# Kernel optimization log

Hardware: AMD Instinct MI355X
Metric: run time of the kernel (lower is better)

The kernel has to match this reference:

```python
import jax, jax.numpy as jnp
import numpy as np

DROPOUT_RATE = 0.5
CONF_THRESH = 0.85
IGNORE_VALUE = 2
EPS = 1e-07


def setup_inputs() -> dict:
    key = jax.random.key(0)
    k1, k2 = jax.random.split(key)
    B, H, W = 16, 1024, 1024
    pred = jax.random.uniform(k1, (B, H, W), dtype=jnp.float32)
    mask = jax.random.randint(k2, (B, H, W), 0, 3, dtype=jnp.int32)
    return {"pred": pred, "mask": mask}


def _training_need_score(pred, gt, confidence):
    # Higher = needs more training: CW=4, UW=3, UC=2, CC=1 (+/- confidence bonus)
    is_correct = (pred > 0.5) == (gt == 1.0)
    is_conf = confidence > CONF_THRESH
    score = jnp.where(is_conf & is_correct, 1.0,
            jnp.where(~is_conf & is_correct, 2.0,
            jnp.where(~is_conf & ~is_correct, 3.0, 4.0))).astype(pred.dtype)
    bonus = (confidence - 0.5) * 0.5
    return jnp.where(is_correct, score - bonus, score + bonus)


def _dynamic_masks(pred, mask):
    # Vectorized equivalent of the per-batch nonzero/argsort/scatter loop:
    # rank annotated pixels per batch by descending need-score; top n_train -> train.
    B, H, W = mask.shape
    annotated = (mask != IGNORE_VALUE).reshape(B, H * W)
    gt = mask.astype(pred.dtype)
    confidence = jnp.maximum(pred, 1.0 - pred)
    scores = _training_need_score(pred, gt, confidence).reshape(B, H * W)
    neg_inf = jnp.asarray(-jnp.inf, scores.dtype)
    masked_scores = jnp.where(annotated, scores, neg_inf)
    order = jnp.argsort(-masked_scores, axis=1)          # descending score order
    rank = jnp.argsort(order, axis=1)                    # rank of each pixel in that order
    n_points = annotated.sum(axis=1)
    n_train = (n_points.astype(jnp.float32) * (1.0 - DROPOUT_RATE)).astype(jnp.int32)
    train = annotated & (rank < n_train[:, None])
    holdout = annotated & ~train
    return train.reshape(B, H, W), holdout.reshape(B, H, W)


def reference(pred, mask):
    if pred.ndim == 4 and pred.shape[1] == 1:
        pred = pred[:, 0]
    train_mask, holdout_mask = _dynamic_masks(pred, mask)
    gt = mask.astype(pred.dtype)
    p = jnp.clip(pred, EPS, 1.0 - EPS)
    bce = -(gt * jnp.log(p) + (1.0 - gt) * jnp.log(1.0 - p))
    tm = train_mask.astype(pred.dtype)
    loss = (bce * tm).sum() / (tm.sum() + EPS)
    return loss, train_mask, holdout_mask
```

## Files before the change

kernel.cpp:

```cpp
#include <hip/hip_runtime.h>
#include <stdint.h>

#define NBATCH 16
#define HW_ (1 << 20)
#define TPB 256

#define NBPB_H 32
#define TPB_H 1024
#define EPB_H (HW_ / NBPB_H)
#define ITER_H (EPB_H / (TPB_H * 4))

#define NBINS 8192
#define FBASE 0x3F400

#define TPB_RF 1024

#define NBPB_F 256
#define FCHUNK (HW_ / NBPB_F)

#define CAND_CAP 32768
#define LCAP 512
#define TIE_CAP 4096
#define CNT_STRIDE 64

typedef float f4v __attribute__((ext_vector_type(4)));

struct BParams {
    unsigned int k;
    unsigned int bin1f;
    unsigned int r;
    unsigned int mode;
};

__device__ __forceinline__ unsigned int score_bits(float p, int m) {
    bool correct = (p > 0.5f) == (m == 1);
    float conf = fmaxf(p, 1.0f - p);
    float base = correct ? ((conf > 0.85f) ? 1.0f : 2.0f)
                         : ((conf > 0.85f) ? 4.0f : 3.0f);
    float bonus = (conf - 0.5f) * 0.5f;
    float s = correct ? (base - bonus) : (base + bonus);
    return __float_as_uint(s);
}

__device__ __forceinline__ float agent_load_f32(const float* p) {
    return __hip_atomic_load(p, __ATOMIC_RELAXED, __HIP_MEMORY_SCOPE_AGENT);
}

__global__ void k_hist1(const float4* __restrict__ pred4, const int4* __restrict__ mask4,
                        unsigned int* __restrict__ hist_part16) {
    __shared__ unsigned int lh[NBINS];
    int b = blockIdx.x / NBPB_H;
    int blk = blockIdx.x % NBPB_H;
    int t = threadIdx.x;
    for (int i = t; i < NBINS; i += TPB_H) lh[i] = 0;
    __syncthreads();
    size_t gb = (size_t)b * (HW_ / 4) + (size_t)blk * (EPB_H / 4);
    float4 p = pred4[gb + t];
    int4 m = mask4[gb + t];
#pragma unroll
    for (int j = 0; j < ITER_H; j++) {
        float4 pc = p;
        int4 mc = m;
        if (j + 1 < ITER_H) {
            p = pred4[gb + (size_t)(j + 1) * TPB_H + t];
            m = mask4[gb + (size_t)(j + 1) * TPB_H + t];
        }
        float pa[4] = {pc.x, pc.y, pc.z, pc.w};
        int ma[4] = {mc.x, mc.y, mc.z, mc.w};
#pragma unroll
        for (int l = 0; l < 4; l++) {
            if (ma[l] != 2) {
                unsigned int sb = score_bits(pa[l], ma[l]);
                int fb = (int)(sb >> 12) - FBASE;
                fb = min(max(fb, 0), NBINS - 1);
                atomicAdd(&lh[fb], 1u);
            }
        }
    }
    __syncthreads();
    unsigned int* hp = hist_part16 + (size_t)(b * NBPB_H + blk) * (NBINS / 2);
    for (int w = t; w < NBINS / 2; w += TPB_H)
        hp[w] = (lh[2 * w] & 0xFFFFu) | (lh[2 * w + 1] << 16);
}

__global__ void k_redfind(const unsigned int* __restrict__ hist_part16,
                          BParams* __restrict__ prm) {
    int b = blockIdx.x;
    int t = threadIdx.x;
    __shared__ unsigned int cs_[TPB_RF + 1];
    unsigned int c[8];
#pragma unroll
    for (int j = 0; j < 8; j++) c[j] = 0;
#pragma unroll
    for (int p = 0; p < NBPB_H; p++) {
        const uint4* hp = (const uint4*)(hist_part16 + (size_t)(b * NBPB_H + p) * (NBINS / 2));
        uint4 w = hp[t];
        c[0] += w.x & 0xFFFFu; c[1] += w.x >> 16;
        c[2] += w.y & 0xFFFFu; c[3] += w.y >> 16;
        c[4] += w.z & 0xFFFFu; c[5] += w.z >> 16;
        c[6] += w.w & 0xFFFFu; c[7] += w.w >> 16;
    }
    unsigned int s = 0;
#pragma unroll
    for (int j = 0; j < 8; j++) s += c[j];
    cs_[t] = s;
    if (t == 0) cs_[TPB_RF] = 0;
    __syncthreads();
    for (int off = 1; off < TPB_RF; off <<= 1) {
        unsigned int a = (t + off < TPB_RF) ? cs_[t + off] : 0u;
        __syncthreads();
        cs_[t] += a;
        __syncthreads();
    }
    unsigned int n = cs_[0];
    unsigned int k = (unsigned int)(int)((float)n * 0.5f);
    if (k == 0) {
        if (t == 0) {
            BParams P;
            P.k = 0; P.bin1f = 0xFFFFFFFFu; P.r = 0; P.mode = 0;
            prm[b] = P;
        }
        return;
    }
    if (cs_[t] >= k && cs_[t + 1] < k) {
        unsigned int cum = cs_[t + 1];
#pragma unroll
        for (int j = 7; j >= 0; j--) {
            unsigned int hb = c[j];
            if (cum + hb >= k) {
                BParams P;
                P.k = k;
                P.bin1f = (unsigned int)(FBASE + t * 8 + j);
                P.r = k - cum;
                P.mode = 1;
                prm[b] = P;
                break;
            }
            cum += hb;
        }
    }
}

__global__ void k_main(const float4* __restrict__ pred4, const int4* __restrict__ mask4,
                       const BParams* __restrict__ prm, float* __restrict__ out,
                       float* __restrict__ partials, unsigned int* __restrict__ cand_cnt,
                       unsigned int* __restrict__ cand_idx, unsigned int* __restrict__ cand_sb,
                       float* __restrict__ cand_bce) {
    int b = blockIdx.x / NBPB_F;
    int blk = blockIdx.x % NBPB_F;
    BParams P = prm[b];
    unsigned int target = P.bin1f;
    __shared__ unsigned int lcode[FCHUNK / 4];
    __shared__ float red[TPB];
    __shared__ unsigned int l_idx[LCAP];
    __shared__ unsigned int l_sb[LCAP];
    __shared__ float l_bce[LCAP];
    __shared__ unsigned int lcnt;
    __shared__ unsigned int gbase;
    if (threadIdx.x == 0) lcnt = 0;
    __syncthreads();
    float acc = 0.0f;
    int ibase = blk * FCHUNK;
    size_t base4 = (size_t)b * (HW_ / 4) + (size_t)(ibase / 4);
    float* trout = out + 1;
    float* hoout = out + 1 + (size_t)NBATCH * HW_;
    size_t Gbase = (size_t)b * HW_ + (size_t)ibase;
    int lane = threadIdx.x & 63;
    float4 p = pred4[base4 + threadIdx.x];
    int4 m = mask4[base4 + threadIdx.x];
#pragma unroll
    for (int j = 0; j < FCHUNK / (TPB * 4); j++) {
        int v = j * TPB + threadIdx.x;
        float4 pc = p;
        int4 mc = m;
        if (j + 1 < FCHUNK / (TPB * 4)) {
            p = pred4[base4 + (size_t)(j + 1) * TPB + threadIdx.x];
            m = mask4[base4 + (size_t)(j + 1) * TPB + threadIdx.x];
        }
        float pa[4] = {pc.x, pc.y, pc.z, pc.w};
        int ma[4] = {mc.x, mc.y, mc.z, mc.w};
        unsigned int cw = 0;
#pragma unroll
        for (int l = 0; l < 4; l++) {
            bool ann = (ma[l] != 2);
            unsigned int sb = score_bits(pa[l], ma[l]);
            unsigned int fine = sb >> 12;
            bool tr = ann && (fine > target);
            bool amb = ann && (fine == target);
            unsigned int code = (tr ? 1u : 0u) | ((ann && !tr) ? 2u : 0u);
            cw |= code << (8 * l);
            float bce = 0.0f;
            if (tr || amb) {
                float pc2 = fminf(fmaxf(pa[l], 1e-7f), 1.0f - 1e-7f);
                bce = (ma[l] == 1) ? -__logf(pc2) : -__logf(1.0f - pc2);
            }
            if (tr) acc += bce;
            if (amb) {
                unsigned int p0 = atomicAdd(&lcnt, 1u);
                if (p0 < LCAP) {
                    l_idx[p0] = (unsigned int)(ibase + v * 4 + l);
                    l_sb[p0] = sb;
                    l_bce[p0] = bce;
                } else {
                    unsigned int gp = atomicAdd(&cand_cnt[b * CNT_STRIDE], 1u);
                    if (gp < CAND_CAP) {
                        size_t o = (size_t)b * CAND_CAP + gp;
                        cand_idx[o] = (unsigned int)(ibase + v * 4 + l);
                        cand_sb[o] = sb;
                        cand_bce[o] = bce;
                    }
                }
            }
        }
        lcode[v] = cw;
        unsigned int nw = (unsigned int)__shfl_down((int)cw, 1);
        if (lane != 63) {
            unsigned int c0 = cw >> 24;
            unsigned int c1 = nw & 0xFFu;
            unsigned int c2 = (nw >> 8) & 0xFFu;
            unsigned int c3 = (nw >> 16) & 0xFFu;
            int e = 3 + 4 * v;
            f4v tv = { (float)(c0 & 1u), (float)(c1 & 1u), (float)(c2 & 1u), (float)(c3 & 1u) };
            f4v hv = { (float)((c0 >> 1) & 1u), (float)((c1 >> 1) & 1u),
                       (float)((c2 >> 1) & 1u), (float)((c3 >> 1) & 1u) };
            *(f4v*)(trout + Gbase + e) = tv;
            *(f4v*)(hoout + Gbase + e) = hv;
        }
    }
    __syncthreads();
    unsigned int n = min(lcnt, (unsigned int)LCAP);
    if (threadIdx.x == 0 && n > 0)
        gbase = atomicAdd(&cand_cnt[b * CNT_STRIDE], n);
    __syncthreads();
    for (unsigned int i = threadIdx.x; i < n; i += TPB) {
        unsigned int pos = gbase + i;
        if (pos < CAND_CAP) {
            size_t o = (size_t)b * CAND_CAP + pos;
            cand_idx[o] = l_idx[i];
            cand_sb[o] = l_sb[i];
            cand_bce[o] = l_bce[i];
        }
    }
    if (threadIdx.x < 16) {
        int j = threadIdx.x >> 2, w = threadIdx.x & 3;
        int v = j * TPB + w * 64 + 63;
        if (v < FCHUNK / 4 - 1) {
            unsigned int w0 = lcode[v];
            unsigned int w1 = lcode[v + 1];
            unsigned int c0 = w0 >> 24;
            unsigned int c1 = w1 & 0xFFu;
            unsigned int c2 = (w1 >> 8) & 0xFFu;
            unsigned int c3 = (w1 >> 16) & 0xFFu;
            int e = 3 + 4 * v;
            f4v tv = { (float)(c0 & 1u), (float)(c1 & 1u), (float)(c2 & 1u), (float)(c3 & 1u) };
            f4v hv = { (float)((c0 >> 1) & 1u), (float)((c1 >> 1) & 1u),
                       (float)((c2 >> 1) & 1u), (float)((c3 >> 1) & 1u) };
            *(f4v*)(trout + Gbase + e) = tv;
            *(f4v*)(hoout + Gbase + e) = hv;
        }
    }
    if (threadIdx.x >= 16 && threadIdx.x < 19) {
        int i = threadIdx.x - 16;
        unsigned int c = (lcode[0] >> (8 * i)) & 0xFFu;
        trout[Gbase + i] = (float)(c & 1u);
        hoout[Gbase + i] = (float)((c >> 1) & 1u);
    }
    if (threadIdx.x == 19) {
        unsigned int c = (lcode[FCHUNK / 4 - 1] >> 24) & 0xFFu;
        trout[Gbase + FCHUNK - 1] = (float)(c & 1u);
        hoout[Gbase + FCHUNK - 1] = (float)((c >> 1) & 1u);
    }
    red[threadIdx.x] = acc;
    __syncthreads();
    for (int off = TPB / 2; off > 0; off >>= 1) {
        if (threadIdx.x < off) red[threadIdx.x] += red[threadIdx.x + off];
        __syncthreads();
    }
    if (threadIdx.x == 0) partials[blockIdx.x] = red[0];
}

__global__ void k_fixup(const unsigned int* __restrict__ cand_cnt,
                        const unsigned int* __restrict__ cand_idx,
                        const unsigned int* __restrict__ cand_sb,
                        const float* __restrict__ cand_bce,
                        const BParams* __restrict__ prm, float* __restrict__ out,
                        float* __restrict__ tie_partials,
                        const float* __restrict__ partials,
                        unsigned int* __restrict__ done_f) {
    int b = blockIdx.x;
    int t = threadIdx.x;
    __shared__ unsigned int h[4096];
    __shared__ unsigned int cs_[257];
    __shared__ unsigned int tie_idx[TIE_CAP];
    __shared__ unsigned int misc[8];
    __shared__ float red[TPB];
    __shared__ double redd[TPB];
    __shared__ unsigned int lastf;
    BParams P = prm[b];
    float tieval = 0.0f;
    if (P.mode != 0) {
        unsigned int C = cand_cnt[b * CNT_STRIDE];
        if (C > CAND_CAP) C = CAND_CAP;
        const unsigned int* ci = cand_idx + (size_t)b * CAND_CAP;
        const unsigned int* cs = cand_sb + (size_t)b * CAND_CAP;
        const float* cb = cand_bce + (size_t)b * CAND_CAP;
        for (int i = t; i < 4096; i += TPB) h[i] = 0;
        if (t < 8) misc[t] = (t == 4) ? 0xFFFFFFFFu : 0u;
        __syncthreads();
        for (unsigned int i = t; i < C; i += TPB)
            atomicAdd(&h[cs[i] & 0xFFFu], 1u);
        __syncthreads();
        {
            unsigned int gs = 0;
#pragma unroll
            for (int j = 0; j < 16; j++) gs += h[t * 16 + j];
            cs_[t] = gs;
            if (t == 0) cs_[256] = 0;
        }
        __syncthreads();
        for (int off = 1; off < 256; off <<= 1) {
            unsigned int a = (t + off < 256) ? cs_[t + off] : 0u;
            __syncthreads();
            cs_[t] += a;
            __syncthreads();
        }
        if (cs_[t] >= P.r && cs_[t + 1] < P.r) {
            unsigned int cum = cs_[t + 1];
            for (int j = 15; j >= 0; j--) {
                unsigned int hb = h[t * 16 + j];
                if (cum + hb >= P.r) {
                    unsigned int T = P.r - cum;
                    misc[0] = (unsigned int)(t * 16 + j);
                    misc[1] = T;
                    misc[2] = (T == hb) ? 1u : 0u;
                    break;
                }
                cum += hb;
            }
        }
        __syncthreads();
        unsigned int vstar = misc[0], T = misc[1];
        bool allTies = (misc[2] != 0);
        unsigned int idxcut;
        if (allTies) {
            idxcut = 0xFFFFFFFFu;
        } else {
            for (unsigned int i = t; i < C; i += TPB) {
                if ((cs[i] & 0xFFFu) == vstar) {
                    unsigned int p = atomicAdd(&misc[3], 1u);
                    if (p < TIE_CAP) tie_idx[p] = ci[i];
                }
            }
            __syncthreads();
            unsigned int E2 = misc[3];
            if (E2 > TIE_CAP) E2 = TIE_CAP;
            for (unsigned int i = t; i < E2; i += TPB) {
                unsigned int vi = tie_idx[i];
                unsigned int cnt = 0;
                for (unsigned int j = 0; j < E2; j++) cnt += (tie_idx[j] < vi) ? 1u : 0u;
                if (cnt == T - 1) misc[4] = vi;
            }
            __syncthreads();
            idxcut = misc[4];
        }
        float acc = 0.0f;
        float* trout = out + 1;
        float* hoout = out + 1 + (size_t)NBATCH * HW_;
        size_t base = (size_t)b * HW_;
        for (unsigned int i = t; i < C; i += TPB) {
            unsigned int low = cs[i] & 0xFFFu;
            bool tr = (low > vstar) || (low == vstar && ci[i] <= idxcut);
            if (tr) {
                trout[base + ci[i]] = 1.0f;
                hoout[base + ci[i]] = 0.0f;
                acc += cb[i];
            }
        }
        red[t] = acc;
        __syncthreads();
        for (int off = TPB / 2; off > 0; off >>= 1) {
            if (t < off) red[t] += red[t + off];
            __syncthreads();
        }
        if (t == 0) tieval = red[0];
    }
    if (t == 0)
        __hip_atomic_store(&tie_partials[b], tieval, __ATOMIC_RELAXED, __HIP_MEMORY_SCOPE_AGENT);
    __threadfence();
    __syncthreads();
    if (t == 0) lastf = (atomicAdd(done_f, 1u) == (unsigned int)(NBATCH - 1)) ? 1u : 0u;
    __syncthreads();
    if (!lastf) return;
    __threadfence();
    double s = 0.0;
    for (int i = t; i < NBATCH * NBPB_F; i += TPB) s += (double)partials[i];
    if (t < NBATCH) s += (double)agent_load_f32(&tie_partials[t]);
    redd[t] = s;
    __syncthreads();
    for (int off = TPB / 2; off > 0; off >>= 1) {
        if (t < off) redd[t] += redd[t + off];
        __syncthreads();
    }
    if (t == 0) {
        unsigned long long den = 0;
        for (int b2 = 0; b2 < NBATCH; b2++) den += prm[b2].k;
        float denf = (float)den + 1e-7f;
        out[0] = (float)redd[0] / denf;
    }
}

extern "C" void kernel_launch(void* const* d_in, const int* in_sizes, int n_in,
                              void* d_out, int out_size, void* d_ws, size_t ws_size,
                              hipStream_t stream) {
    const float4* pred4 = (const float4*)d_in[0];
    const int4* mask4 = (const int4*)d_in[1];
    float* out = (float*)d_out;

    unsigned int* cand_cnt = (unsigned int*)d_ws;
    unsigned int* done_f = cand_cnt + NBATCH * CNT_STRIDE;
    BParams* prm = (BParams*)(done_f + 32);
    float* partials = (float*)(prm + NBATCH);
    float* tie_partials = partials + NBATCH * NBPB_F;
    unsigned int* cand_idx = (unsigned int*)(tie_partials + NBATCH);
    unsigned int* cand_sb = cand_idx + NBATCH * CAND_CAP;
    float* cand_bce = (float*)(cand_sb + NBATCH * CAND_CAP);
    unsigned int* hist_part16 = (unsigned int*)(cand_bce + NBATCH * CAND_CAP);

    size_t zero_bytes = (size_t)(NBATCH * CNT_STRIDE + 32) * 4;
    hipMemsetAsync(d_ws, 0, zero_bytes, stream);

    k_hist1<<<dim3(NBATCH * NBPB_H), dim3(TPB_H), 0, stream>>>(pred4, mask4, hist_part16);
    k_redfind<<<dim3(NBATCH), dim3(TPB_RF), 0, stream>>>(hist_part16, prm);
    k_main<<<dim3(NBATCH * NBPB_F), dim3(TPB), 0, stream>>>(pred4, mask4, prm, out, partials,
                                                            cand_cnt, cand_idx, cand_sb, cand_bce);
    k_fixup<<<dim3(NBATCH), dim3(TPB), 0, stream>>>(cand_cnt, cand_idx, cand_sb, cand_bce,
                                                    prm, out, tie_partials, partials, done_f);
}
```

Measured before the change: 295.4 us.

## Fuse four kernel launches into one cooperative persistent kernel with grid syncs

Merges the histogram, threshold-finding, main masking, and tie fixup kernels into one cooperative kernel of 512 blocks with 512 threads, separated by grid.sync barriers. The histogram reduction is parallelized across slices, and the memset is replaced by in-kernel zeroing. This aims to remove launch gaps and the memset. It reduces the main-pass grid from 4096 blocks to 512 and adds several grid-wide barriers, which can hurt latency hiding.

```diff
diff --git a/kernel.cpp b/kernel.cpp
--- a/kernel.cpp
+++ b/kernel.cpp
@@ -1,27 +1,28 @@
 #include <hip/hip_runtime.h>
+#include <hip/hip_cooperative_groups.h>
 #include <stdint.h>
+
+namespace cg = cooperative_groups;
 
 #define NBATCH 16
 #define HW_ (1 << 20)
-#define TPB 256
-
-#define NBPB_H 32
-#define TPB_H 1024
-#define EPB_H (HW_ / NBPB_H)
-#define ITER_H (EPB_H / (TPB_H * 4))
+#define NB 512
+#define TPBC 512
+#define NBPB 32
+#define EPB (HW_ / NBPB)
+#define ITER_P (EPB / (TPBC * 4))
 
 #define NBINS 8192
 #define FBASE 0x3F400
-
-#define TPB_RF 1024
-
-#define NBPB_F 256
-#define FCHUNK (HW_ / NBPB_F)
+#define NSLICE 32
+#define SLICE_BINS 256
 
 #define CAND_CAP 32768
 #define LCAP 512
 #define TIE_CAP 4096
 #define CNT_STRIDE 64
+
+#define BUF_W 10242
 
 typedef float f4v __attribute__((ext_vector_type(4)));
 
@@ -42,209 +43,212 @@
     return __float_as_uint(s);
 }
 
-__device__ __forceinline__ float agent_load_f32(const float* p) {
-    return __hip_atomic_load(p, __ATOMIC_RELAXED, __HIP_MEMORY_SCOPE_AGENT);
-}
-
-__global__ void k_hist1(const float4* __restrict__ pred4, const int4* __restrict__ mask4,
-                        unsigned int* __restrict__ hist_part16) {
-    __shared__ unsigned int lh[NBINS];
-    int b = blockIdx.x / NBPB_H;
-    int blk = blockIdx.x % NBPB_H;
-    int t = threadIdx.x;
-    for (int i = t; i < NBINS; i += TPB_H) lh[i] = 0;
+__global__ __launch_bounds__(TPBC, 4) void k_all(
+    const float4* __restrict__ pred4, const int4* __restrict__ mask4,
+    float* __restrict__ out,
+    unsigned int* __restrict__ cand_cnt, BParams* __restrict__ prm,
+    float* __restrict__ partials, float* __restrict__ tie_partials,
+    unsigned int* __restrict__ cand_idx, unsigned int* __restrict__ cand_sb,
+    float* __restrict__ cand_bce, unsigned int* __restrict__ hist1,
+    unsigned int* __restrict__ stot, unsigned int* __restrict__ hist_part16)
+{
+    cg::grid_group grid = cg::this_grid();
+    __shared__ __align__(16) unsigned int buf[BUF_W];
+    const int blk = blockIdx.x;
+    const int t = threadIdx.x;
+    const int b = blk / NBPB;
+    const int sb = blk % NBPB;
+    const int lane = t & 63;
+
+    for (int i = t; i < NBINS; i += TPBC) buf[i] = 0;
+    if (blk == 0)
+        for (int i = t; i < NBATCH * CNT_STRIDE; i += TPBC) cand_cnt[i] = 0;
     __syncthreads();
-    size_t gb = (size_t)b * (HW_ / 4) + (size_t)blk * (EPB_H / 4);
-    float4 p = pred4[gb + t];
-    int4 m = mask4[gb + t];
+    {
+        size_t gb = (size_t)b * (HW_ / 4) + (size_t)sb * (EPB / 4);
+        float4 p = pred4[gb + t];
+        int4 m = mask4[gb + t];
+        for (int j = 0; j < ITER_P; j++) {
+            float4 pc = p; int4 mc = m;
+            if (j + 1 < ITER_P) {
+                p = pred4[gb + (size_t)(j + 1) * TPBC + t];
+                m = mask4[gb + (size_t)(j + 1) * TPBC + t];
+            }
+            float pa[4] = {pc.x, pc.y, pc.z, pc.w};
+            int   ma[4] = {mc.x, mc.y, mc.z, mc.w};
 #pragma unroll
-    for (int j = 0; j < ITER_H; j++) {
-        float4 pc = p;
-        int4 mc = m;
-        if (j + 1 < ITER_H) {
-            p = pred4[gb + (size_t)(j + 1) * TPB_H + t];
-            m = mask4[gb + (size_t)(j + 1) * TPB_H + t];
-        }
-        float pa[4] = {pc.x, pc.y, pc.z, pc.w};
-        int ma[4] = {mc.x, mc.y, mc.z, mc.w};
-#pragma unroll
-        for (int l = 0; l < 4; l++) {
-            if (ma[l] != 2) {
-                unsigned int sb = score_bits(pa[l], ma[l]);
-                int fb = (int)(sb >> 12) - FBASE;
-                fb = min(max(fb, 0), NBINS - 1);
-                atomicAdd(&lh[fb], 1u);
+            for (int l = 0; l < 4; l++) {
+                if (ma[l] != 2) {
+                    unsigned int sbit = score_bits(pa[l], ma[l]);
+                    int fb = (int)(sbit >> 12) - FBASE;
+                    fb = min(max(fb, 0), NBINS - 1);
+                    atomicAdd(&buf[fb], 1u);
+                }
             }
         }
     }
     __syncthreads();
-    unsigned int* hp = hist_part16 + (size_t)(b * NBPB_H + blk) * (NBINS / 2);
-    for (int w = t; w < NBINS / 2; w += TPB_H)
-        hp[w] = (lh[2 * w] & 0xFFFFu) | (lh[2 * w + 1] << 16);
-}
-
-__global__ void k_redfind(const unsigned int* __restrict__ hist_part16,
-                          BParams* __restrict__ prm) {
-    int b = blockIdx.x;
-    int t = threadIdx.x;
-    __shared__ unsigned int cs_[TPB_RF + 1];
-    unsigned int c[8];
-#pragma unroll
-    for (int j = 0; j < 8; j++) c[j] = 0;
-#pragma unroll
-    for (int p = 0; p < NBPB_H; p++) {
-        const uint4* hp = (const uint4*)(hist_part16 + (size_t)(b * NBPB_H + p) * (NBINS / 2));
-        uint4 w = hp[t];
-        c[0] += w.x & 0xFFFFu; c[1] += w.x >> 16;
-        c[2] += w.y & 0xFFFFu; c[3] += w.y >> 16;
-        c[4] += w.z & 0xFFFFu; c[5] += w.z >> 16;
-        c[6] += w.w & 0xFFFFu; c[7] += w.w >> 16;
-    }
-    unsigned int s = 0;
-#pragma unroll
-    for (int j = 0; j < 8; j++) s += c[j];
-    cs_[t] = s;
-    if (t == 0) cs_[TPB_RF] = 0;
+    {
+        unsigned int* hp = hist_part16 + (size_t)blk * (NBINS / 2);
+        for (int w = t; w < NBINS / 2; w += TPBC)
+            hp[w] = (buf[2 * w] & 0xFFFFu) | (buf[2 * w + 1] << 16);
+    }
+    grid.sync();
+
+    if (t < 128) {
+        unsigned int s0 = 0, s1 = 0;
+        for (int p = 0; p < NBPB; p++) {
+            unsigned int w = hist_part16[(size_t)(b * NBPB + p) * (NBINS / 2) + sb * 128 + t];
+            s0 += w & 0xFFFFu; s1 += w >> 16;
+        }
+        hist1[(size_t)b * NBINS + sb * SLICE_BINS + 2 * t] = s0;
+        hist1[(size_t)b * NBINS + sb * SLICE_BINS + 2 * t + 1] = s1;
+        buf[t] = s0 + s1;
+    }
     __syncthreads();
-    for (int off = 1; off < TPB_RF; off <<= 1) {
-        unsigned int a = (t + off < TPB_RF) ? cs_[t + off] : 0u;
-        __syncthreads();
-        cs_[t] += a;
-        __syncthreads();
-    }
-    unsigned int n = cs_[0];
-    unsigned int k = (unsigned int)(int)((float)n * 0.5f);
-    if (k == 0) {
+    for (int off = 64; off > 0; off >>= 1) {
+        if (t < off) buf[t] += buf[t + off];
+        __syncthreads();
+    }
+    if (t == 0) stot[b * NBPB + sb] = buf[0];
+    grid.sync();
+
+    if (sb == 0) {
+        if (t < NSLICE) buf[256 + t] = stot[b * NBPB + t];
+        __syncthreads();
         if (t == 0) {
-            BParams P;
-            P.k = 0; P.bin1f = 0xFFFFFFFFu; P.r = 0; P.mode = 0;
-            prm[b] = P;
-        }
-        return;
-    }
-    if (cs_[t] >= k && cs_[t + 1] < k) {
-        unsigned int cum = cs_[t + 1];
-#pragma unroll
-        for (int j = 7; j >= 0; j--) {
-            unsigned int hb = c[j];
-            if (cum + hb >= k) {
-                BParams P;
-                P.k = k;
-                P.bin1f = (unsigned int)(FBASE + t * 8 + j);
-                P.r = k - cum;
+            unsigned int run = 0;
+            for (int i = NSLICE - 1; i >= 0; i--) { run += buf[256 + i]; buf[288 + i] = run; }
+            buf[320] = run;
+        }
+        __syncthreads();
+        unsigned int n = buf[320];
+        unsigned int k = (unsigned int)(int)((float)n * 0.5f);
+        if (k == 0) {
+            if (t == 0) { BParams P; P.k = 0; P.bin1f = 0xFFFFFFFFu; P.r = 0; P.mode = 0; prm[b] = P; }
+        } else {
+            if (t == 0) {
+                int ss = 0;
+                for (int i = NSLICE - 1; i >= 0; i--) {
+                    unsigned int sufi = buf[288 + i];
+                    unsigned int sufn = (i == NSLICE - 1) ? 0u : buf[288 + i + 1];
+                    if (sufi >= k && sufn < k) { ss = i; break; }
+                }
+                buf[321] = (unsigned int)ss;
+                buf[322] = k - ((ss == NSLICE - 1) ? 0u : buf[288 + ss + 1]);
+            }
+            __syncthreads();
+            unsigned int ss = buf[321], rs = buf[322];
+            if (t < SLICE_BINS) buf[512 + t] = hist1[(size_t)b * NBINS + ss * SLICE_BINS + t];
+            if (t == 0) buf[512 + SLICE_BINS] = 0;
+            __syncthreads();
+            for (int off = 1; off < SLICE_BINS; off <<= 1) {
+                unsigned int a = (t < SLICE_BINS && t + off < SLICE_BINS) ? buf[512 + t + off] : 0u;
+                __syncthreads();
+                if (t < SLICE_BINS) buf[512 + t] += a;
+                __syncthreads();
+            }
+            if (t < SLICE_BINS && buf[512 + t] >= rs && buf[512 + t + 1] < rs) {
+                BParams P; P.k = k;
+                P.bin1f = (unsigned int)(FBASE + ss * SLICE_BINS + t);
+                P.r = rs - buf[512 + t + 1];
                 P.mode = 1;
                 prm[b] = P;
-                break;
-            }
-            cum += hb;
-        }
-    }
-}
-
-__global__ void k_main(const float4* __restrict__ pred4, const int4* __restrict__ mask4,
-                       const BParams* __restrict__ prm, float* __restrict__ out,
-                       float* __restrict__ partials, unsigned int* __restrict__ cand_cnt,
-                       unsigned int* __restrict__ cand_idx, unsigned int* __restrict__ cand_sb,
-                       float* __restrict__ cand_bce) {
-    int b = blockIdx.x / NBPB_F;
-    int blk = blockIdx.x % NBPB_F;
-    BParams P = prm[b];
-    unsigned int target = P.bin1f;
-    __shared__ unsigned int lcode[FCHUNK / 4];
-    __shared__ float red[TPB];
-    __shared__ unsigned int l_idx[LCAP];
-    __shared__ unsigned int l_sb[LCAP];
-    __shared__ float l_bce[LCAP];
-    __shared__ unsigned int lcnt;
-    __shared__ unsigned int gbase;
-    if (threadIdx.x == 0) lcnt = 0;
-    __syncthreads();
-    float acc = 0.0f;
-    int ibase = blk * FCHUNK;
-    size_t base4 = (size_t)b * (HW_ / 4) + (size_t)(ibase / 4);
-    float* trout = out + 1;
-    float* hoout = out + 1 + (size_t)NBATCH * HW_;
-    size_t Gbase = (size_t)b * HW_ + (size_t)ibase;
-    int lane = threadIdx.x & 63;
-    float4 p = pred4[base4 + threadIdx.x];
-    int4 m = mask4[base4 + threadIdx.x];
+            }
+        }
+    }
+    grid.sync();
+
+    {
+        unsigned int* lcode = buf;
+        unsigned int* l_idx = buf + 8192;
+        unsigned int* l_sbv = buf + 8704;
+        float*        l_bce = (float*)(buf + 9216);
+        float*        redf  = (float*)(buf + 9728);
+        BParams P = prm[b];
+        unsigned int target = P.bin1f;
+        if (t == 0) buf[10240] = 0;
+        __syncthreads();
+        float acc = 0.0f;
+        int ibase = sb * EPB;
+        size_t base4 = (size_t)b * (HW_ / 4) + (size_t)(ibase / 4);
+        float* trout = out + 1;
+        float* hoout = out + 1 + (size_t)NBATCH * HW_;
+        size_t Gbase = (size_t)b * HW_ + (size_t)ibase;
+        float4 p = pred4[base4 + t];
+        int4 m = mask4[base4 + t];
+        for (int j = 0; j < ITER_P; j++) {
+            int v = j * TPBC + t;
+            float4 pc = p; int4 mc = m;
+            if (j + 1 < ITER_P) {
+                p = pred4[base4 + (size_t)(j + 1) * TPBC + t];
+                m = mask4[base4 + (size_t)(j + 1) * TPBC + t];
+            }
+            float pa[4] = {pc.x, pc.y, pc.z, pc.w};
+            int   ma[4] = {mc.x, mc.y, mc.z, mc.w};
+            unsigned int cw = 0;
 #pragma unroll
-    for (int j = 0; j < FCHUNK / (TPB * 4); j++) {
-        int v = j * TPB + threadIdx.x;
-        float4 pc = p;
-        int4 mc = m;
-        if (j + 1 < FCHUNK / (TPB * 4)) {
-            p = pred4[base4 + (size_t)(j + 1) * TPB + threadIdx.x];
-            m = mask4[base4 + (size_t)(j + 1) * TPB + threadIdx.x];
-        }
-        float pa[4] = {pc.x, pc.y, pc.z, pc.w};
-        int ma[4] = {mc.x, mc.y, mc.z, mc.w};
-        unsigned int cw = 0;
-#pragma unroll
-        for (int l = 0; l < 4; l++) {
-            bool ann = (ma[l] != 2);
-            unsigned int sb = score_bits(pa[l], ma[l]);
-            unsigned int fine = sb >> 12;
-            bool tr = ann && (fine > target);
-            bool amb = ann && (fine == target);
-            unsigned int code = (tr ? 1u : 0u) | ((ann && !tr) ? 2u : 0u);
-            cw |= code << (8 * l);
-            float bce = 0.0f;
-            if (tr || amb) {
-                float pc2 = fminf(fmaxf(pa[l], 1e-7f), 1.0f - 1e-7f);
-                bce = (ma[l] == 1) ? -__logf(pc2) : -__logf(1.0f - pc2);
-            }
-            if (tr) acc += bce;
-            if (amb) {
-                unsigned int p0 = atomicAdd(&lcnt, 1u);
-                if (p0 < LCAP) {
-                    l_idx[p0] = (unsigned int)(ibase + v * 4 + l);
-                    l_sb[p0] = sb;
-                    l_bce[p0] = bce;
-                } else {
-                    unsigned int gp = atomicAdd(&cand_cnt[b * CNT_STRIDE], 1u);
-                    if (gp < CAND_CAP) {
-                        size_t o = (size_t)b * CAND_CAP + gp;
-                        cand_idx[o] = (unsigned int)(ibase + v * 4 + l);
-                        cand_sb[o] = sb;
-                        cand_bce[o] = bce;
+            for (int l = 0; l < 4; l++) {
+                bool ann = (ma[l] != 2);
+                unsigned int sbit = score_bits(pa[l], ma[l]);
+                unsigned int fine = sbit >> 12;
+                bool tr = ann && (fine > target);
+                bool amb = ann && (fine == target);
+                unsigned int code = (tr ? 1u : 0u) | ((ann && !tr) ? 2u : 0u);
+                cw |= code << (8 * l);
+                float bce = 0.0f;
+                if (tr || amb) {
+                    float pc2 = fminf(fmaxf(pa[l], 1e-7f), 1.0f - 1e-7f);
+                    bce = (ma[l] == 1) ? -__logf(pc2) : -__logf(1.0f - pc2);
+                }
+                if (tr) acc += bce;
+                if (amb) {
+                    unsigned int p0 = atomicAdd(&buf[10240], 1u);
+                    if (p0 < LCAP) {
+                        l_idx[p0] = (unsigned int)(ibase + v * 4 + l);
+                        l_sbv[p0] = sbit;
+                        l_bce[p0] = bce;
+                    } else {
+                        unsigned int gp = atomicAdd(&cand_cnt[b * CNT_STRIDE], 1u);
+                        if (gp < CAND_CAP) {
+                            size_t o = (size_t)b * CAND_CAP + gp;
+                            cand_idx[o] = (unsigned int)(ibase + v * 4 + l);
+                            cand_sb[o] = sbit;
+                            cand_bce[o] = bce;
+                        }
                     }
                 }
             }
-        }
-        lcode[v] = cw;
-        unsigned int nw = (unsigned int)__shfl_down((int)cw, 1);
-        if (lane != 63) {
-            unsigned int c0 = cw >> 24;
-            unsigned int c1 = nw & 0xFFu;
-            unsigned int c2 = (nw >> 8) & 0xFFu;
-            unsigned int c3 = (nw >> 16) & 0xFFu;
-            int e = 3 + 4 * v;
-            f4v tv = { (float)(c0 & 1u), (float)(c1 & 1u), (float)(c2 & 1u), (float)(c3 & 1u) };
-            f4v hv = { (float)((c0 >> 1) & 1u), (float)((c1 >> 1) & 1u),
-                       (float)((c2 >> 1) & 1u), (float)((c3 >> 1) & 1u) };
-            *(f4v*)(trout + Gbase + e) = tv;
-            *(f4v*)(hoout + Gbase + e) = hv;
-        }
-    }
-    __syncthreads();
-    unsigned int n = min(lcnt, (unsigned int)LCAP);
-    if (threadIdx.x == 0 && n > 0)
-        gbase = atomicAdd(&cand_cnt[b * CNT_STRIDE], n);
-    __syncthreads();
-    for (unsigned int i = threadIdx.x; i < n; i += TPB) {
-        unsigned int pos = gbase + i;
-        if (pos < CAND_CAP) {
-            size_t o = (size_t)b * CAND_CAP + pos;
-            cand_idx[o] = l_idx[i];
-            cand_sb[o] = l_sb[i];
-            cand_bce[o] = l_bce[i];
-        }
-    }
-    if (threadIdx.x < 16) {
-        int j = threadIdx.x >> 2, w = threadIdx.x & 3;
-        int v = j * TPB + w * 64 + 63;
-        if (v < FCHUNK / 4 - 1) {
+            lcode[v] = cw;
+            unsigned int nw = (unsigned int)__shfl_down((int)cw, 1);
+            if (lane != 63) {
+                unsigned int c0 = cw >> 24;
+                unsigned int c1 = nw & 0xFFu;
+                unsigned int c2 = (nw >> 8) & 0xFFu;
+                unsigned int c3 = (nw >> 16) & 0xFFu;
+                int e = 3 + 4 * v;
+                f4v tv = { (float)(c0 & 1u), (float)(c1 & 1u), (float)(c2 & 1u), (float)(c3 & 1u) };
+                f4v hv = { (float)((c0 >> 1) & 1u), (float)((c1 >> 1) & 1u),
+                           (float)((c2 >> 1) & 1u), (float)((c3 >> 1) & 1u) };
+                *(f4v*)(trout + Gbase + e) = tv;
+                *(f4v*)(hoout + Gbase + e) = hv;
+            }
+        }
+        __syncthreads();
+        unsigned int ncand = min(buf[10240], (unsigned int)LCAP);
+        if (t == 0 && ncand > 0) buf[10241] = atomicAdd(&cand_cnt[b * CNT_STRIDE], ncand);
+        __syncthreads();
+        for (unsigned int i = t; i < ncand; i += TPBC) {
+            unsigned int pos = buf[10241] + i;
+            if (pos < CAND_CAP) {
+                size_t o = (size_t)b * CAND_CAP + pos;
+                cand_idx[o] = l_idx[i];
+                cand_sb[o] = l_sbv[i];
+                cand_bce[o] = l_bce[i];
+            }
+        }
+        if (t < 127) {
+            int v = t * 64 + 63;
             unsigned int w0 = lcode[v];
             unsigned int w1 = lcode[v + 1];
             unsigned int c0 = w0 >> 24;
@@ -258,154 +262,140 @@
             *(f4v*)(trout + Gbase + e) = tv;
             *(f4v*)(hoout + Gbase + e) = hv;
         }
-    }
-    if (threadIdx.x >= 16 && threadIdx.x < 19) {
-        int i = threadIdx.x - 16;
-        unsigned int c = (lcode[0] >> (8 * i)) & 0xFFu;
-        trout[Gbase + i] = (float)(c & 1u);
-        hoout[Gbase + i] = (float)((c >> 1) & 1u);
-    }
-    if (threadIdx.x == 19) {
-        unsigned int c = (lcode[FCHUNK / 4 - 1] >> 24) & 0xFFu;
-        trout[Gbase + FCHUNK - 1] = (float)(c & 1u);
-        hoout[Gbase + FCHUNK - 1] = (float)((c >> 1) & 1u);
-    }
-    red[threadIdx.x] = acc;
-    __syncthreads();
-    for (int off = TPB / 2; off > 0; off >>= 1) {
-        if (threadIdx.x < off) red[threadIdx.x] += red[threadIdx.x + off];
-        __syncthreads();
-    }
-    if (threadIdx.x == 0) partials[blockIdx.x] = red[0];
-}
-
-__global__ void k_fixup(const unsigned int* __restrict__ cand_cnt,
-                        const unsigned int* __restrict__ cand_idx,
-                        const unsigned int* __restrict__ cand_sb,
-                        const float* __restrict__ cand_bce,
-                        const BParams* __restrict__ prm, float* __restrict__ out,
-                        float* __restrict__ tie_partials,
-                        const float* __restrict__ partials,
-                        unsigned int* __restrict__ done_f) {
-    int b = blockIdx.x;
-    int t = threadIdx.x;
-    __shared__ unsigned int h[4096];
-    __shared__ unsigned int cs_[257];
-    __shared__ unsigned int tie_idx[TIE_CAP];
-    __shared__ unsigned int misc[8];
-    __shared__ float red[TPB];
-    __shared__ double redd[TPB];
-    __shared__ unsigned int lastf;
-    BParams P = prm[b];
-    float tieval = 0.0f;
-    if (P.mode != 0) {
-        unsigned int C = cand_cnt[b * CNT_STRIDE];
-        if (C > CAND_CAP) C = CAND_CAP;
-        const unsigned int* ci = cand_idx + (size_t)b * CAND_CAP;
-        const unsigned int* cs = cand_sb + (size_t)b * CAND_CAP;
-        const float* cb = cand_bce + (size_t)b * CAND_CAP;
-        for (int i = t; i < 4096; i += TPB) h[i] = 0;
-        if (t < 8) misc[t] = (t == 4) ? 0xFFFFFFFFu : 0u;
-        __syncthreads();
-        for (unsigned int i = t; i < C; i += TPB)
-            atomicAdd(&h[cs[i] & 0xFFFu], 1u);
-        __syncthreads();
-        {
-            unsigned int gs = 0;
+        if (t >= 128 && t < 131) {
+            int i = t - 128;
+            unsigned int c = (lcode[0] >> (8 * i)) & 0xFFu;
+            trout[Gbase + i] = (float)(c & 1u);
+            hoout[Gbase + i] = (float)((c >> 1) & 1u);
+        }
+        if (t == 131) {
+            unsigned int c = (lcode[EPB / 4 - 1] >> 24) & 0xFFu;
+            trout[Gbase + EPB - 1] = (float)(c & 1u);
+            hoout[Gbase + EPB - 1] = (float)((c >> 1) & 1u);
+        }
+        redf[t] = acc;
+        __syncthreads();
+        for (int off = TPBC / 2; off > 0; off >>= 1) {
+            if (t < off) redf[t] += redf[t + off];
+            __syncthreads();
+        }
+        if (t == 0) partials[blk] = redf[0];
+    }
+    grid.sync();
+
+    if (sb == 0) {
+        unsigned int* h    = buf;
+        unsigned int* csx  = buf + 4096;
+        unsigned int* tie  = buf + 4609;
+        unsigned int* misc = buf + 8705;
+        float* redf = (float*)(buf + 8713);
+        BParams P = prm[b];
+        if (P.mode == 0) {
+            if (t == 0) tie_partials[b] = 0.0f;
+        } else {
+            unsigned int C = cand_cnt[b * CNT_STRIDE];
+            if (C > CAND_CAP) C = CAND_CAP;
+            const unsigned int* ci = cand_idx + (size_t)b * CAND_CAP;
+            const unsigned int* cs = cand_sb + (size_t)b * CAND_CAP;
+            const float* cb = cand_bce + (size_t)b * CAND_CAP;
+            for (int i = t; i < 4096; i += TPBC) h[i] = 0;
+            if (t < 8) misc[t] = (t == 4) ? 0xFFFFFFFFu : 0u;
+            __syncthreads();
+            for (unsigned int i = t; i < C; i += TPBC)
+                atomicAdd(&h[cs[i] & 0xFFFu], 1u);
+            __syncthreads();
+            {
+                unsigned int gs = 0;
 #pragma unroll
-            for (int j = 0; j < 16; j++) gs += h[t * 16 + j];
-            cs_[t] = gs;
-            if (t == 0) cs_[256] = 0;
-        }
-        __syncthreads();
-        for (int off = 1; off < 256; off <<= 1) {
-            unsigned int a = (t + off < 256) ? cs_[t + off] : 0u;
-            __syncthreads();
-            cs_[t] += a;
-            __syncthreads();
-        }
-        if (cs_[t] >= P.r && cs_[t + 1] < P.r) {
-            unsigned int cum = cs_[t + 1];
-            for (int j = 15; j >= 0; j--) {
-                unsigned int hb = h[t * 16 + j];
-                if (cum + hb >= P.r) {
-                    unsigned int T = P.r - cum;
-                    misc[0] = (unsigned int)(t * 16 + j);
-                    misc[1] = T;
-                    misc[2] = (T == hb) ? 1u : 0u;
-                    break;
-                }
-                cum += hb;
-            }
-        }
-        __syncthreads();
-        unsigned int vstar = misc[0], T = misc[1];
-        bool allTies = (misc[2] != 0);
-        unsigned int idxcut;
-        if (allTies) {
-            idxcut = 0xFFFFFFFFu;
-        } else {
-            for (unsigned int i = t; i < C; i += TPB) {
-                if ((cs[i] & 0xFFFu) == vstar) {
-                    unsigned int p = atomicAdd(&misc[3], 1u);
-                    if (p < TIE_CAP) tie_idx[p] = ci[i];
-                }
-            }
-            __syncthreads();
-            unsigned int E2 = misc[3];
-            if (E2 > TIE_CAP) E2 = TIE_CAP;
-            for (unsigned int i = t; i < E2; i += TPB) {
-                unsigned int vi = tie_idx[i];
-                unsigned int cnt = 0;
-                for (unsigned int j = 0; j < E2; j++) cnt += (tie_idx[j] < vi) ? 1u : 0u;
-                if (cnt == T - 1) misc[4] = vi;
-            }
-            __syncthreads();
-            idxcut = misc[4];
-        }
-        float acc = 0.0f;
-        float* trout = out + 1;
-        float* hoout = out + 1 + (size_t)NBATCH * HW_;
-        size_t base = (size_t)b * HW_;
-        for (unsigned int i = t; i < C; i += TPB) {
-            unsigned int low = cs[i] & 0xFFFu;
-            bool tr = (low > vstar) || (low == vstar && ci[i] <= idxcut);
-            if (tr) {
-                trout[base + ci[i]] = 1.0f;
-                hoout[base + ci[i]] = 0.0f;
-                acc += cb[i];
-            }
-        }
-        red[t] = acc;
-        __syncthreads();
-        for (int off = TPB / 2; off > 0; off >>= 1) {
-            if (t < off) red[t] += red[t + off];
-            __syncthreads();
-        }
-        if (t == 0) tieval = red[0];
-    }
-    if (t == 0)
-        __hip_atomic_store(&tie_partials[b], tieval, __ATOMIC_RELAXED, __HIP_MEMORY_SCOPE_AGENT);
-    __threadfence();
-    __syncthreads();
-    if (t == 0) lastf = (atomicAdd(done_f, 1u) == (unsigned int)(NBATCH - 1)) ? 1u : 0u;
-    __syncthreads();
-    if (!lastf) return;
-    __threadfence();
-    double s = 0.0;
-    for (int i = t; i < NBATCH * NBPB_F; i += TPB) s += (double)partials[i];
-    if (t < NBATCH) s += (double)agent_load_f32(&tie_partials[t]);
-    redd[t] = s;
-    __syncthreads();
-    for (int off = TPB / 2; off > 0; off >>= 1) {
-        if (t < off) redd[t] += redd[t + off];
-        __syncthreads();
-    }
-    if (t == 0) {
-        unsigned long long den = 0;
-        for (int b2 = 0; b2 < NBATCH; b2++) den += prm[b2].k;
-        float denf = (float)den + 1e-7f;
-        out[0] = (float)redd[0] / denf;
+                for (int j = 0; j < 8; j++) gs += h[t * 8 + j];
+                csx[t] = gs;
+                if (t == 0) csx[TPBC] = 0;
+            }
+            __syncthreads();
+            for (int off = 1; off < TPBC; off <<= 1) {
+                unsigned int a = (t + off < TPBC) ? csx[t + off] : 0u;
+                __syncthreads();
+                csx[t] += a;
+                __syncthreads();
+            }
+            if (csx[t] >= P.r && csx[t + 1] < P.r) {
+                unsigned int cum = csx[t + 1];
+                for (int j = 7; j >= 0; j--) {
+                    unsigned int hb = h[t * 8 + j];
+                    if (cum + hb >= P.r) {
+                        unsigned int T = P.r - cum;
+                        misc[0] = (unsigned int)(t * 8 + j);
+                        misc[1] = T;
+                        misc[2] = (T == hb) ? 1u : 0u;
+                        break;
+                    }
+                    cum += hb;
+                }
+            }
+            __syncthreads();
+            unsigned int vstar = misc[0], T = misc[1];
+            bool allTies = (misc[2] != 0);
+            unsigned int idxcut;
+            if (allTies) {
+                idxcut = 0xFFFFFFFFu;
+            } else {
+                for (unsigned int i = t; i < C; i += TPBC) {
+                    if ((cs[i] & 0xFFFu) == vstar) {
+                        unsigned int p0 = atomicAdd(&misc[3], 1u);
+                        if (p0 < TIE_CAP) tie[p0] = ci[i];
+                    }
+                }
+                __syncthreads();
+                unsigned int E2 = misc[3];
+                if (E2 > TIE_CAP) E2 = TIE_CAP;
+                for (unsigned int i = t; i < E2; i += TPBC) {
+                    unsigned int vi = tie[i];
+                    unsigned int cnt = 0;
+                    for (unsigned int j2 = 0; j2 < E2; j2++) cnt += (tie[j2] < vi) ? 1u : 0u;
+                    if (cnt == T - 1) misc[4] = vi;
+                }
+                __syncthreads();
+                idxcut = misc[4];
+            }
+            float accd = 0.0f;
+            float* trout = out + 1;
+            float* hoout = out + 1 + (size_t)NBATCH * HW_;
+            size_t baseo = (size_t)b * HW_;
+            for (unsigned int i = t; i < C; i += TPBC) {
+                unsigned int low = cs[i] & 0xFFFu;
+                bool tr = (low > vstar) || (low == vstar && ci[i] <= idxcut);
+                if (tr) {
+                    trout[baseo + ci[i]] = 1.0f;
+                    hoout[baseo + ci[i]] = 0.0f;
+                    accd += cb[i];
+                }
+            }
+            redf[t] = accd;
+            __syncthreads();
+            for (int off = TPBC / 2; off > 0; off >>= 1) {
+                if (t < off) redf[t] += redf[t + off];
+                __syncthreads();
+            }
+            if (t == 0) tie_partials[b] = redf[0];
+        }
+    }
+    grid.sync();
+
+    if (blk == 0) {
+        double* redd = (double*)buf;
+        double s = (double)partials[t];
+        if (t < NBATCH) s += (double)tie_partials[t];
+        redd[t] = s;
+        __syncthreads();
+        for (int off = TPBC / 2; off > 0; off >>= 1) {
+            if (t < off) redd[t] += redd[t + off];
+            __syncthreads();
+        }
+        if (t == 0) {
+            unsigned long long den = 0;
+            for (int b2 = 0; b2 < NBATCH; b2++) den += prm[b2].k;
+            out[0] = (float)redd[0] / ((float)den + 1e-7f);
+        }
     }
 }
 
@@ -417,22 +407,19 @@
     float* out = (float*)d_out;
 
     unsigned int* cand_cnt = (unsigned int*)d_ws;
-    unsigned int* done_f = cand_cnt + NBATCH * CNT_STRIDE;
-    BParams* prm = (BParams*)(done_f + 32);
+    BParams* prm = (BParams*)(cand_cnt + NBATCH * CNT_STRIDE);
     float* partials = (float*)(prm + NBATCH);
-    float* tie_partials = partials + NBATCH * NBPB_F;
-    unsigned int* cand_idx = (unsigned int*)(tie_partials + NBATCH);
+    float* tie_partials = partials + NB;
+    unsigned int* stot = (unsigned int*)(tie_partials + NBATCH);
+    unsigned int* cand_idx = stot + NB;
     unsigned int* cand_sb = cand_idx + NBATCH * CAND_CAP;
     float* cand_bce = (float*)(cand_sb + NBATCH * CAND_CAP);
-    unsigned int* hist_part16 = (unsigned int*)(cand_bce + NBATCH * CAND_CAP);
-
-    size_t zero_bytes = (size_t)(NBATCH * CNT_STRIDE + 32) * 4;
-    hipMemsetAsync(d_ws, 0, zero_bytes, stream);
-
-    k_hist1<<<dim3(NBATCH * NBPB_H), dim3(TPB_H), 0, stream>>>(pred4, mask4, hist_part16);
-    k_redfind<<<dim3(NBATCH), dim3(TPB_RF), 0, stream>>>(hist_part16, prm);
-    k_main<<<dim3(NBATCH * NBPB_F), dim3(TPB), 0, stream>>>(pred4, mask4, prm, out, partials,
-                                                            cand_cnt, cand_idx, cand_sb, cand_bce);
-    k_fixup<<<dim3(NBATCH), dim3(TPB), 0, stream>>>(cand_cnt, cand_idx, cand_sb, cand_bce,
-                                                    prm, out, tie_partials, partials, done_f);
+    unsigned int* hist1 = (unsigned int*)(cand_bce + NBATCH * CAND_CAP);
+    unsigned int* hist_part16 = hist1 + NBATCH * NBINS;
+
+    void* args[] = { (void*)&pred4, (void*)&mask4, (void*)&out, (void*)&cand_cnt,
+                     (void*)&prm, (void*)&partials, (void*)&tie_partials,
+                     (void*)&cand_idx, (void*)&cand_sb, (void*)&cand_bce,
+                     (void*)&hist1, (void*)&stot, (void*)&hist_part16 };
+    hipLaunchCooperativeKernel((const void*)k_all, dim3(NB), dim3(TPBC), args, 0, stream);
 }
```

New measurement: 564.8 us. 1.91x slower.

## Split histogram reduce/find into parallel kernels and retune histogram blocks

Applied to the files above, without the earlier changes.

Doubles the number of histogram blocks per batch and halves their size, with a launch bound and a two-deep load prefetch. The former single-block-per-batch reduce-and-scan kernel becomes a sliced reduction kernel with 64 blocks plus a smaller 256-thread find kernel that scans the reduced histogram. The aim is to spread the partial-histogram reduction over more CUs and raise occupancy in the histogram pass. The cost is an extra kernel launch, twice as many partial histograms to write and read, and a serial 32-bin scan in the find step.

```diff
diff --git a/kernel.cpp b/kernel.cpp
--- a/kernel.cpp
+++ b/kernel.cpp
@@ -5,15 +5,16 @@
 #define HW_ (1 << 20)
 #define TPB 256
 
-#define NBPB_H 32
-#define TPB_H 1024
+#define NBPB_H 64
+#define TPB_H 512
 #define EPB_H (HW_ / NBPB_H)
 #define ITER_H (EPB_H / (TPB_H * 4))
 
 #define NBINS 8192
 #define FBASE 0x3F400
 
-#define TPB_RF 1024
+#define NSLICE 4
+#define SLICE_W (NBINS / 2 / NSLICE)
 
 #define NBPB_F 256
 #define FCHUNK (HW_ / NBPB_F)
@@ -46,8 +47,9 @@
     return __hip_atomic_load(p, __ATOMIC_RELAXED, __HIP_MEMORY_SCOPE_AGENT);
 }
 
-__global__ void k_hist1(const float4* __restrict__ pred4, const int4* __restrict__ mask4,
-                        unsigned int* __restrict__ hist_part16) {
+__global__ __launch_bounds__(TPB_H, 8) void k_hist1(
+        const float4* __restrict__ pred4, const int4* __restrict__ mask4,
+        unsigned int* __restrict__ hist_part16) {
     __shared__ unsigned int lh[NBINS];
     int b = blockIdx.x / NBPB_H;
     int blk = blockIdx.x % NBPB_H;
@@ -55,16 +57,7 @@
     for (int i = t; i < NBINS; i += TPB_H) lh[i] = 0;
     __syncthreads();
     size_t gb = (size_t)b * (HW_ / 4) + (size_t)blk * (EPB_H / 4);
-    float4 p = pred4[gb + t];
-    int4 m = mask4[gb + t];
-#pragma unroll
-    for (int j = 0; j < ITER_H; j++) {
-        float4 pc = p;
-        int4 mc = m;
-        if (j + 1 < ITER_H) {
-            p = pred4[gb + (size_t)(j + 1) * TPB_H + t];
-            m = mask4[gb + (size_t)(j + 1) * TPB_H + t];
-        }
+    auto process = [&](float4 pc, int4 mc) {
         float pa[4] = {pc.x, pc.y, pc.z, pc.w};
         int ma[4] = {mc.x, mc.y, mc.z, mc.w};
 #pragma unroll
@@ -76,6 +69,25 @@
                 atomicAdd(&lh[fb], 1u);
             }
         }
+    };
+    float4 p0 = pred4[gb + t];
+    int4 m0 = mask4[gb + t];
+    float4 p1 = pred4[gb + TPB_H + t];
+    int4 m1 = mask4[gb + TPB_H + t];
+#pragma unroll
+    for (int jj = 0; jj < ITER_H; jj += 2) {
+        float4 pc0 = p0; int4 mc0 = m0;
+        if (jj + 2 < ITER_H) {
+            p0 = pred4[gb + (size_t)(jj + 2) * TPB_H + t];
+            m0 = mask4[gb + (size_t)(jj + 2) * TPB_H + t];
+        }
+        process(pc0, mc0);
+        float4 pc1 = p1; int4 mc1 = m1;
+        if (jj + 3 < ITER_H) {
+            p1 = pred4[gb + (size_t)(jj + 3) * TPB_H + t];
+            m1 = mask4[gb + (size_t)(jj + 3) * TPB_H + t];
+        }
+        process(pc1, mc1);
     }
     __syncthreads();
     unsigned int* hp = hist_part16 + (size_t)(b * NBPB_H + blk) * (NBINS / 2);
@@ -83,31 +95,40 @@
         hp[w] = (lh[2 * w] & 0xFFFFu) | (lh[2 * w + 1] << 16);
 }
 
-__global__ void k_redfind(const unsigned int* __restrict__ hist_part16,
-                          BParams* __restrict__ prm) {
+__global__ void k_reduce(const unsigned int* __restrict__ hist_part16,
+                         unsigned int* __restrict__ hist1) {
+    int b = blockIdx.x / NSLICE;
+    int sl = blockIdx.x % NSLICE;
+    int t = threadIdx.x;
+    int w = sl * SLICE_W + t;
+    unsigned int s0 = 0, s1 = 0;
+#pragma unroll 8
+    for (int p = 0; p < NBPB_H; p++) {
+        unsigned int v = hist_part16[(size_t)(b * NBPB_H + p) * (NBINS / 2) + w];
+        s0 += v & 0xFFFFu;
+        s1 += v >> 16;
+    }
+    uint2* ob = (uint2*)(hist1 + (size_t)b * NBINS + 2 * (size_t)w);
+    uint2 o = {s0, s1};
+    *ob = o;
+}
+
+__global__ void k_find1(const unsigned int* __restrict__ hist1, BParams* prm) {
     int b = blockIdx.x;
     int t = threadIdx.x;
-    __shared__ unsigned int cs_[TPB_RF + 1];
-    unsigned int c[8];
-#pragma unroll
-    for (int j = 0; j < 8; j++) c[j] = 0;
-#pragma unroll
-    for (int p = 0; p < NBPB_H; p++) {
-        const uint4* hp = (const uint4*)(hist_part16 + (size_t)(b * NBPB_H + p) * (NBINS / 2));
-        uint4 w = hp[t];
-        c[0] += w.x & 0xFFFFu; c[1] += w.x >> 16;
-        c[2] += w.y & 0xFFFFu; c[3] += w.y >> 16;
-        c[4] += w.z & 0xFFFFu; c[5] += w.z >> 16;
-        c[6] += w.w & 0xFFFFu; c[7] += w.w >> 16;
-    }
-    unsigned int s = 0;
-#pragma unroll
-    for (int j = 0; j < 8; j++) s += c[j];
-    cs_[t] = s;
-    if (t == 0) cs_[TPB_RF] = 0;
-    __syncthreads();
-    for (int off = 1; off < TPB_RF; off <<= 1) {
-        unsigned int a = (t + off < TPB_RF) ? cs_[t + off] : 0u;
+    __shared__ unsigned int cs_[257];
+    const unsigned int* h = hist1 + (size_t)b * NBINS;
+    {
+        const uint4* h4 = (const uint4*)(h + t * 32);
+        unsigned int s = 0;
+#pragma unroll
+        for (int j = 0; j < 8; j++) { uint4 v = h4[j]; s += v.x + v.y + v.z + v.w; }
+        cs_[t] = s;
+        if (t == 0) cs_[256] = 0;
+    }
+    __syncthreads();
+    for (int off = 1; off < 256; off <<= 1) {
+        unsigned int a = (t + off < 256) ? cs_[t + off] : 0u;
         __syncthreads();
         cs_[t] += a;
         __syncthreads();
@@ -124,13 +145,12 @@
     }
     if (cs_[t] >= k && cs_[t + 1] < k) {
         unsigned int cum = cs_[t + 1];
-#pragma unroll
-        for (int j = 7; j >= 0; j--) {
-            unsigned int hb = c[j];
+        for (int j = 31; j >= 0; j--) {
+            unsigned int hb = h[t * 32 + j];
             if (cum + hb >= k) {
                 BParams P;
                 P.k = k;
-                P.bin1f = (unsigned int)(FBASE + t * 8 + j);
+                P.bin1f = (unsigned int)(FBASE + t * 32 + j);
                 P.r = k - cum;
                 P.mode = 1;
                 prm[b] = P;
@@ -424,13 +444,15 @@
     unsigned int* cand_idx = (unsigned int*)(tie_partials + NBATCH);
     unsigned int* cand_sb = cand_idx + NBATCH * CAND_CAP;
     float* cand_bce = (float*)(cand_sb + NBATCH * CAND_CAP);
-    unsigned int* hist_part16 = (unsigned int*)(cand_bce + NBATCH * CAND_CAP);
+    unsigned int* hist1 = (unsigned int*)(cand_bce + NBATCH * CAND_CAP);
+    unsigned int* hist_part16 = hist1 + NBATCH * NBINS;
 
     size_t zero_bytes = (size_t)(NBATCH * CNT_STRIDE + 32) * 4;
     hipMemsetAsync(d_ws, 0, zero_bytes, stream);
 
     k_hist1<<<dim3(NBATCH * NBPB_H), dim3(TPB_H), 0, stream>>>(pred4, mask4, hist_part16);
-    k_redfind<<<dim3(NBATCH), dim3(TPB_RF), 0, stream>>>(hist_part16, prm);
+    k_reduce<<<dim3(NBATCH * NSLICE), dim3(1024), 0, stream>>>(hist_part16, hist1);
+    k_find1<<<dim3(NBATCH), dim3(TPB), 0, stream>>>(hist1, prm);
     k_main<<<dim3(NBATCH * NBPB_F), dim3(TPB), 0, stream>>>(pred4, mask4, prm, out, partials,
                                                             cand_cnt, cand_idx, cand_sb, cand_bce);
     k_fixup<<<dim3(NBATCH), dim3(TPB), 0, stream>>>(cand_cnt, cand_idx, cand_sb, cand_bce,
```

After: 299.3 us. About the same (+1.3%).
